# Kernel tuning notes

Measured on AMD Instinct MI355X. Metric: run time of the kernel, lower is better.

Reference implementation:

```python
import jax, jax.numpy as jnp
import numpy as np

B, S, D = 4, 8192, 512
WS = 512        # window_size
LB = 1          # look_backward (look_forward = 0, causal)


def setup_inputs() -> dict:
    key = jax.random.key(0)
    k1, k2, k3 = jax.random.split(key, 3)
    text = jax.random.normal(k1, (B, S, D), dtype=jnp.float32)
    audio = jax.random.normal(k2, (B, S, D), dtype=jnp.float32)
    video = jax.random.normal(k3, (B, S, D), dtype=jnp.float32)
    return {"text": text, "audio": audio, "video": video}


def _local_attention(q, k, v, ws=WS, lb=LB):
    # q, k, v: [b, n, d]; sliding-window causal attention, each query window
    # attends to its own window plus `lb` previous windows.
    b, n, d = q.shape
    w = n // ws
    scale = d ** -0.5
    qw = q.reshape(b, w, ws, d) * scale
    kw = k.reshape(b, w, ws, d)
    vw = v.reshape(b, w, ws, d)

    def look_around(x):
        # pad lb windows of zeros at the front, gather lb+1 shifted views
        padded = jnp.pad(x, ((0, 0), (lb, 0), (0, 0), (0, 0)))
        return jnp.concatenate([padded[:, i:i + w] for i in range(lb + 1)], axis=2)

    kk = look_around(kw)  # [b, w, (lb+1)*ws, d]
    vv = look_around(vw)

    # absolute positions for causal + padding mask
    t = jnp.arange(n).reshape(w, ws)                        # query positions [w, ws]
    tk = jnp.pad(t, ((lb, 0), (0, 0)), constant_values=-1)  # pad windows get -1
    bq_k = jnp.concatenate([tk[i:i + w] for i in range(lb + 1)], axis=1)  # [w, (lb+1)*ws]
    mask = (t[:, :, None] >= bq_k[:, None, :]) & (bq_k[:, None, :] >= 0)  # [w, ws, (lb+1)*ws]

    sim = jnp.einsum('bwid,bwjd->bwij', qw, kk)             # [b, w, ws, (lb+1)*ws]
    sim = jnp.where(mask[None], sim, jnp.finfo(sim.dtype).min)
    attn = jax.nn.softmax(sim, axis=-1)
    out = jnp.einsum('bwij,bwjd->bwid', attn, vv)
    return out.reshape(b, n, d)


def reference(text, audio, video):
    # GATSBlock.forward: x = self.local_attn(text, audio, video)
    # i.e. q = text, k = audio, v = video (modalities pre-projected to [b, n, d])
    return _local_attention(text, audio, video)
```

## Files before the change

kernel.cpp:

```cpp
#include <hip/hip_runtime.h>
#include <hip/hip_bf16.h>

#define S_ 8192
#define D_ 512
#define WSZ 512
#define QBLK 64
#define KBLK 32
#define ATT_THREADS 256
#define PSTRIDE 2560
#define ATT_LDS (65536 + 2 * PSTRIDE)

using bf16x8 = __attribute__((ext_vector_type(8))) __bf16;
using f32x4  = __attribute__((ext_vector_type(4))) float;
using f32x16 = __attribute__((ext_vector_type(16))) float;

#define GLDS(gp, lp) __builtin_amdgcn_global_load_lds( \
    (const __attribute__((address_space(1))) void*)(gp), \
    (__attribute__((address_space(3))) void*)(lp), 16, 0, 0)

__global__ __launch_bounds__(256) void cvt_k(const float* __restrict__ in,
                                             ushort* __restrict__ out) {
    const int bid = blockIdx.x;
    const int j = bid & 7, t = (bid >> 3) & 255, b = bid >> 11;
    const int u = j * 256 + threadIdx.x;
    const int c = u >> 7, row = (u >> 2) & 31, h = u & 3;
    const float* src = in + ((size_t)(b * S_ + t * 32 + row)) * D_ + c * 32 + h * 8;
    float4 a0 = *(const float4*)(src);
    float4 a1 = *(const float4*)(src + 4);
    bf16x8 o;
    o[0] = (__bf16)a0.x; o[1] = (__bf16)a0.y; o[2] = (__bf16)a0.z; o[3] = (__bf16)a0.w;
    o[4] = (__bf16)a1.x; o[5] = (__bf16)a1.y; o[6] = (__bf16)a1.z; o[7] = (__bf16)a1.w;
    *(bf16x8*)(out + (size_t)(b * 256 + t) * 16384 + u * 8) = o;
}

__global__ __launch_bounds__(256) void tr_v(const float* __restrict__ V,
                                            char* __restrict__ Vt) {
    __shared__ float tile[64][68];
    const int bid = blockIdx.x;
    const int d0 = (bid & 7) * 64;
    const int s0 = ((bid >> 3) & 127) * 64;
    const int b  = bid >> 10;
    const int t  = threadIdx.x;
    {
        const int sl = t >> 2, cg = (t & 3) * 16;
        const float* src = V + ((size_t)b * S_ + s0 + sl) * D_ + d0 + cg;
        #pragma unroll
        for (int j = 0; j < 4; ++j)
            *(float4*)&tile[sl][cg + j * 4] = *(const float4*)(src + j * 4);
    }
    __syncthreads();
    {
        const int dl = t >> 2, sg = (t & 3) * 16;
        const int d  = d0 + dl;
        const int tt = (s0 + sg) >> 5;
        const int kk = (s0 + sg) & 31;
        bf16x8 o0, o1;
        #pragma unroll
        for (int j = 0; j < 8; ++j) {
            o0[j] = (__bf16)tile[sg + j][dl];
            o1[j] = (__bf16)tile[sg + 8 + j][dl];
        }
        char* base = Vt + (size_t)(b * 256 + tt) * 32768 +
                     (d >> 5) * 2048 + (d & 31) * 16;
        *(bf16x8*)(base + (kk >> 4) * 1024)       = o0;
        *(bf16x8*)(base + (kk >> 4) * 1024 + 512) = o1;
    }
}

__global__ __launch_bounds__(ATT_THREADS, 2) void gats_attn(
    const float* __restrict__ Qg, const char* __restrict__ Kbg,
    const char* __restrict__ Vtg, float* __restrict__ Og)
{
    extern __shared__ char smem[];
    const int tid  = threadIdx.x;
    const int lane = tid & 63;
    const int wv   = tid >> 6;
    const int h    = lane >> 4;
    const int lq   = lane & 15;
    const int hh   = lane >> 5;
    const int l31  = lane & 31;
    const int u    = wv & 1;
    const int pr   = wv >> 1;
    char* Pp = smem + 65536 + pr * PSTRIDE;
    char* Pf = Pp + 2048;
    const int laneK = lq * 64 + h * 16;

    const int bid = blockIdx.x;
    const int r2  = bid >> 3;
    const int w   = (bid & 7) * 2 + (r2 & 1);
    const int b   = (r2 >> 1) & 3;
    const int y   = r2 >> 3;
    const int qbase    = w * WSZ + y * QBLK;
    const int pairbase = qbase + pr * 32;
    const int wqbase   = qbase + wv * 16;

    const float* Qp  = Qg  + (size_t)b * S_ * D_;
    const char*  Kbp = Kbg + (size_t)b * 256 * 32768;
    const char*  Vtp = Vtg + (size_t)b * 256 * 32768;
    float*       Op  = Og  + (size_t)b * S_ * D_;

    const float scale = 0.044194173824159216f;
    const float L2E   = 1.44269504088896f;

    bf16x8 qf[16];
    {
        const int qrow = wqbase + lq;
        const float* qsrc = Qp + (size_t)qrow * D_ + h * 8;
        #pragma unroll
        for (int c = 0; c < 16; ++c) {
            float4 a0 = *(const float4*)(qsrc + c * 32);
            float4 a1 = *(const float4*)(qsrc + c * 32 + 4);
            bf16x8 q;
            q[0] = (__bf16)(a0.x * scale); q[1] = (__bf16)(a0.y * scale);
            q[2] = (__bf16)(a0.z * scale); q[3] = (__bf16)(a0.w * scale);
            q[4] = (__bf16)(a1.x * scale); q[5] = (__bf16)(a1.y * scale);
            q[6] = (__bf16)(a1.z * scale); q[7] = (__bf16)(a1.w * scale);
            qf[c] = q;
        }
    }

    f32x16 acc[8];
    #pragma unroll
    for (int dt = 0; dt < 8; ++dt)
        #pragma unroll
        for (int rg = 0; rg < 16; ++rg) acc[dt][rg] = 0.f;
    float m_run = -1e30f, l_run = 0.f;

    const int kstart = (w == 0) ? 0 : (w - 1) * WSZ;
    const int ktend  = qbase + QBLK;

    auto STAGE = [&](int kt) {
        char* kb = smem;
        char* vb = smem + 32768;
        const size_t tb = ((size_t)(kt >> 5)) << 15;
        const char* ksrc = Kbp + tb;
        const char* vsrc = Vtp + tb;
        #pragma unroll
        for (int s2 = 0; s2 < 8; ++s2) {
            const int off = wv * 8192 + s2 * 1024;
            GLDS(ksrc + off + lane * 16, kb + off);
            GLDS(vsrc + off + lane * 16, vb + off);
        }
    };

    STAGE(kstart);
    for (int kt = kstart; kt < ktend; kt += KBLK) {
        asm volatile("s_waitcnt vmcnt(0)" ::: "memory");
        __builtin_amdgcn_s_barrier();

        const bool active = (kt <= pairbase + 31);
        char* Ksh = smem;
        char* Vsh = smem + 32768;

        if (active) {
            f32x4 st[2];
            __builtin_amdgcn_s_setprio(1);
            #pragma unroll
            for (int g = 0; g < 2; ++g) {
                f32x4 sa = (f32x4){0.f, 0.f, 0.f, 0.f};
                f32x4 sb = (f32x4){0.f, 0.f, 0.f, 0.f};
                #pragma unroll
                for (int c = 0; c < 16; ++c) {
                    const int byte = c * 2048 + g * 1024 + laneK;
                    bf16x8 kf = *(const bf16x8*)(Ksh + byte);
                    if (c & 1) sb = __builtin_amdgcn_mfma_f32_16x16x32_bf16(kf, qf[c], sb, 0, 0, 0);
                    else       sa = __builtin_amdgcn_mfma_f32_16x16x32_bf16(kf, qf[c], sa, 0, 0, 0);
                }
                st[g] = sa + sb;
            }
            __builtin_amdgcn_s_setprio(0);

            const int qg = wqbase + lq;
            if (kt + 31 > wqbase) {
                #pragma unroll
                for (int g = 0; g < 2; ++g)
                    #pragma unroll
                    for (int r = 0; r < 4; ++r) {
                        const int key = kt + g * 16 + h * 4 + r;
                        if (key > qg) st[g][r] = -1e30f;
                    }
            }

            float own = fmaxf(fmaxf(fmaxf(st[0][0], st[0][1]), fmaxf(st[0][2], st[0][3])),
                              fmaxf(fmaxf(st[1][0], st[1][1]), fmaxf(st[1][2], st[1][3])));
            float tmax = fmaxf(own, __shfl_xor(own, 16));
            tmax = fmaxf(tmax, __shfl_xor(tmax, 32));

            const bool anyneed = __any(tmax > m_run + 8.f);
            float f_val = 1.0f;
            if (anyneed) {
                const float mnew = fmaxf(m_run, tmax);
                f_val = exp2f((m_run - mnew) * L2E);
                m_run = mnew;
                l_run *= f_val;
            }

            const float p00 = exp2f((st[0][0] - m_run) * L2E);
            const float p01 = exp2f((st[0][1] - m_run) * L2E);
            const float p02 = exp2f((st[0][2] - m_run) * L2E);
            const float p03 = exp2f((st[0][3] - m_run) * L2E);
            const float p10 = exp2f((st[1][0] - m_run) * L2E);
            const float p11 = exp2f((st[1][1] - m_run) * L2E);
            const float p12 = exp2f((st[1][2] - m_run) * L2E);
            const float p13 = exp2f((st[1][3] - m_run) * L2E);
            float rs = p00 + p01 + p02 + p03 + p10 + p11 + p12 + p13;
            rs += __shfl_xor(rs, 16);
            rs += __shfl_xor(rs, 32);
            l_run += rs;

            uint c0, c1, c2, c3;
            asm("v_cvt_pk_bf16_f32 %0, %1, %2" : "=v"(c0) : "v"(p00), "v"(p01));
            asm("v_cvt_pk_bf16_f32 %0, %1, %2" : "=v"(c1) : "v"(p02), "v"(p03));
            asm("v_cvt_pk_bf16_f32 %0, %1, %2" : "=v"(c2) : "v"(p10), "v"(p11));
            asm("v_cvt_pk_bf16_f32 %0, %1, %2" : "=v"(c3) : "v"(p12), "v"(p13));
            const int wbase = (h >> 1) * 512 + (h & 1) * 8 + (u * 16 + lq) * 16;
            *(uint*)(Pp + wbase)            = c0;
            *(uint*)(Pp + wbase + 4)        = c1;
            *(uint*)(Pp + 1024 + wbase)     = c2;
            *(uint*)(Pp + 1024 + wbase + 4) = c3;
            if (h == 0)    *(float*)(Pf + (u * 16 + lq) * 4) = f_val;
            if (lane == 0) *(uint*)(Pf + 128 + u * 4) = anyneed ? 1u : 0u;
        }

        asm volatile("s_waitcnt lgkmcnt(0)" ::: "memory");
        __builtin_amdgcn_sched_barrier(0);
        __builtin_amdgcn_s_barrier();

        if (active) {
            const uint2 fl = *(const uint2*)(Pf + 128);
            if (fl.x | fl.y) {
                f32x4 fr[4];
                #pragma unroll
                for (int i = 0; i < 4; ++i)
                    fr[i] = *(const f32x4*)(Pf + i * 32 + hh * 16);
                #pragma unroll
                for (int dt = 0; dt < 8; ++dt)
                    #pragma unroll
                    for (int rg = 0; rg < 16; ++rg)
                        acc[dt][rg] *= fr[rg >> 2][rg & 3];
            }

            bf16x8 pa0 = *(const bf16x8*)(Pp + hh * 512 + l31 * 16);
            bf16x8 pa1 = *(const bf16x8*)(Pp + 1024 + hh * 512 + l31 * 16);
            __builtin_amdgcn_s_setprio(1);
            #pragma unroll
            for (int dt = 0; dt < 8; ++dt) {
                const int vb = (u * 8 + dt) * 2048 + hh * 512 + l31 * 16;
                bf16x8 v0 = *(const bf16x8*)(Vsh + vb);
                bf16x8 v1 = *(const bf16x8*)(Vsh + vb + 1024);
                acc[dt] = __builtin_amdgcn_mfma_f32_32x32x16_bf16(pa0, v0, acc[dt], 0, 0, 0);
                acc[dt] = __builtin_amdgcn_mfma_f32_32x32x16_bf16(pa1, v1, acc[dt], 0, 0, 0);
            }
            __builtin_amdgcn_s_setprio(0);
        }
        __builtin_amdgcn_s_barrier();
        if (kt + KBLK < ktend) STAGE(kt + KBLK);
    }

    if (h == 0) *(float*)(Pf + (u * 16 + lq) * 4) = l_run;
    asm volatile("s_waitcnt lgkmcnt(0)" ::: "memory");
    __builtin_amdgcn_s_barrier();
    f32x4 iv[4];
    #pragma unroll
    for (int i = 0; i < 4; ++i) {
        f32x4 lv = *(const f32x4*)(Pf + i * 32 + hh * 16);
        iv[i][0] = 1.0f / lv[0]; iv[i][1] = 1.0f / lv[1];
        iv[i][2] = 1.0f / lv[2]; iv[i][3] = 1.0f / lv[3];
    }
    #pragma unroll
    for (int dt = 0; dt < 8; ++dt) {
        const int colb = u * 256 + dt * 32 + l31;
        #pragma unroll
        for (int rg = 0; rg < 16; ++rg) {
            const int row = pairbase + (rg & 3) + 8 * (rg >> 2) + 4 * hh;
            Op[(size_t)row * D_ + colb] = acc[dt][rg] * iv[rg >> 2][rg & 3];
        }
    }
}

#define FB_LDS (32768 + 32768 + 4 * 1024)
__global__ __launch_bounds__(256, 2) void gats_attn_fb(
    const float* __restrict__ Qg, const float* __restrict__ Kg,
    const float* __restrict__ Vg, float* __restrict__ Og)
{
    extern __shared__ char smem[];
    char* Ksh = smem;
    char* Vsh = smem + 32768;
    const int tid  = threadIdx.x;
    const int lane = tid & 63;
    const int wv   = tid >> 6;
    char* Psh = smem + 65536 + wv * 1024;
    const int bid = blockIdx.x;
    const int wh  = bid & 7;
    const int r2  = bid >> 3;
    const int w   = wh * 2 + (r2 & 1);
    const int b   = (r2 >> 1) & 3;
    const int y   = r2 >> 3;
    const int qbase  = w * WSZ + y * 64;
    const int wqbase = qbase + wv * 16;
    const size_t boff = (size_t)b * S_ * D_;
    const float* Qp = Qg + boff; const float* Kp = Kg + boff;
    const float* Vp = Vg + boff; float* Op = Og + boff;
    const float scale = 0.044194173824159216f;
    const float L2E   = 1.44269504088896f;
    bf16x8 qf[16];
    {
        const int qrow = wqbase + (lane & 15);
        const float* qsrc = Qp + (size_t)qrow * D_ + ((lane >> 4) * 8);
        #pragma unroll
        for (int c = 0; c < 16; ++c) {
            float4 a0 = *(const float4*)(qsrc + c * 32);
            float4 a1 = *(const float4*)(qsrc + c * 32 + 4);
            bf16x8 q;
            q[0] = (__bf16)(a0.x * scale); q[1] = (__bf16)(a0.y * scale);
            q[2] = (__bf16)(a0.z * scale); q[3] = (__bf16)(a0.w * scale);
            q[4] = (__bf16)(a1.x * scale); q[5] = (__bf16)(a1.y * scale);
            q[6] = (__bf16)(a1.z * scale); q[7] = (__bf16)(a1.w * scale);
            qf[c] = q;
        }
    }
    f32x4 acc[32];
    #pragma unroll
    for (int i = 0; i < 32; ++i) acc[i] = (f32x4){0.f, 0.f, 0.f, 0.f};
    float m_r[4], l_r[4];
    #pragma unroll
    for (int r = 0; r < 4; ++r) { m_r[r] = -1e30f; l_r[r] = 0.f; }
    const int kstart = (w == 0) ? 0 : (w - 1) * WSZ;
    const int ktend  = qbase + 64;
    for (int kt = kstart; kt < ktend; kt += 32) {
        __syncthreads();
        #pragma unroll
        for (int s = 0; s < 8; ++s) {
            const int row = s * 4 + wv;
            const int dof = lane * 8;
            const float4* src = (const float4*)(Kp + (size_t)(kt + row) * D_ + dof);
            float4 a0 = src[0], a1 = src[1];
            bf16x8 kv;
            kv[0] = (__bf16)a0.x; kv[1] = (__bf16)a0.y; kv[2] = (__bf16)a0.z; kv[3] = (__bf16)a0.w;
            kv[4] = (__bf16)a1.x; kv[5] = (__bf16)a1.y; kv[6] = (__bf16)a1.z; kv[7] = (__bf16)a1.w;
            const int byte = row * 1024 + ((dof * 2) ^ ((row & 7) << 4));
            *(bf16x8*)(Ksh + byte) = kv;
        }
        #pragma unroll
        for (int hh2 = 0; hh2 < 2; ++hh2) {
            const int d = tid + hh2 * 256;
            #pragma unroll
            for (int it = 0; it < 4; ++it) {
                float vvv[8];
                #pragma unroll
                for (int j = 0; j < 8; ++j)
                    vvv[j] = Vp[(size_t)(kt + it * 8 + j) * D_ + d];
                bf16x8 vb;
                #pragma unroll
                for (int j = 0; j < 8; ++j) vb[j] = (__bf16)vvv[j];
                const int byte = d * 64 + ((it * 16) ^ (((d >> 1) & 3) << 4));
                *(bf16x8*)(Vsh + byte) = vb;
            }
        }
        __syncthreads();
        if (kt > wqbase + 15) continue;
        f32x4 sacc[2];
        #pragma unroll
        for (int g = 0; g < 2; ++g) {
            f32x4 s = (f32x4){0.f, 0.f, 0.f, 0.f};
            const int keyrow = g * 16 + (lane & 15);
            #pragma unroll
            for (int c = 0; c < 16; ++c) {
                const int byte = keyrow * 1024 +
                                 ((c * 64 + (lane >> 4) * 16) ^ ((keyrow & 7) << 4));
                bf16x8 kf = *(const bf16x8*)(Ksh + byte);
                s = __builtin_amdgcn_mfma_f32_16x16x32_bf16(qf[c], kf, s, 0, 0, 0);
            }
            sacc[g] = s;
        }
        #pragma unroll
        for (int g = 0; g < 2; ++g) {
            if (kt + g * 16 + 15 > wqbase) {
                const int kg = kt + g * 16 + (lane & 15);
                #pragma unroll
                for (int r = 0; r < 4; ++r) {
                    const int qrow = wqbase + (lane >> 4) * 4 + r;
                    if (kg > qrow) sacc[g][r] = -1e30f;
                }
            }
        }
        float tmax[4];
        #pragma unroll
        for (int r = 0; r < 4; ++r) {
            float v = fmaxf(sacc[0][r], sacc[1][r]);
            #pragma unroll
            for (int off = 8; off >= 1; off >>= 1)
                v = fmaxf(v, __shfl_xor(v, off));
            tmax[r] = v;
        }
        bool need = false;
        #pragma unroll
        for (int r = 0; r < 4; ++r) need |= (tmax[r] > m_r[r] + 8.f);
        if (__any(need)) {
            #pragma unroll
            for (int r = 0; r < 4; ++r) {
                const float mnew = fmaxf(m_r[r], tmax[r]);
                const float f = exp2f((m_r[r] - mnew) * L2E);
                m_r[r] = mnew; l_r[r] *= f;
                #pragma unroll
                for (int dc = 0; dc < 32; ++dc) acc[dc][r] *= f;
            }
        }
        float rsum[4] = {0.f, 0.f, 0.f, 0.f};
        #pragma unroll
        for (int g = 0; g < 2; ++g) {
            #pragma unroll
            for (int r = 0; r < 4; ++r) {
                const float p = exp2f((sacc[g][r] - m_r[r]) * L2E);
                rsum[r] += p;
                const int prow = (lane >> 4) * 4 + r;
                const int byte = prow * 64 +
                                 ((g * 32 + (lane & 15) * 2) ^ (((prow >> 1) & 3) << 4));
                *(__bf16*)(Psh + byte) = (__bf16)p;
            }
        }
        #pragma unroll
        for (int r = 0; r < 4; ++r) {
            float v = rsum[r];
            #pragma unroll
            for (int off = 8; off >= 1; off >>= 1)
                v += __shfl_xor(v, off);
            l_r[r] += v;
        }
        {
            const int prow  = lane & 15;
            const int pbyte = prow * 64 +
                              (((lane >> 4) * 16) ^ (((prow >> 1) & 3) << 4));
            bf16x8 pa = *(const bf16x8*)(Psh + pbyte);
            #pragma unroll
            for (int dc = 0; dc < 32; ++dc) {
                const int d = dc * 16 + (lane & 15);
                const int vbyte = d * 64 +
                                  (((lane >> 4) * 16) ^ (((d >> 1) & 3) << 4));
                bf16x8 vf = *(const bf16x8*)(Vsh + vbyte);
                acc[dc] = __builtin_amdgcn_mfma_f32_16x16x32_bf16(pa, vf, acc[dc], 0, 0, 0);
            }
        }
    }
    float inv[4];
    #pragma unroll
    for (int r = 0; r < 4; ++r) inv[r] = 1.0f / l_r[r];
    #pragma unroll
    for (int dc = 0; dc < 32; ++dc) {
        #pragma unroll
        for (int r = 0; r < 4; ++r) {
            const int row = wqbase + (lane >> 4) * 4 + r;
            const int col = dc * 16 + (lane & 15);
            Op[(size_t)row * D_ + col] = acc[dc][r] * inv[r];
        }
    }
}

extern "C" void kernel_launch(void* const* d_in, const int* in_sizes, int n_in,
                              void* d_out, int out_size, void* d_ws, size_t ws_size,
                              hipStream_t stream) {
    const float* q = (const float*)d_in[0];
    const float* k = (const float*)d_in[1];
    const float* v = (const float*)d_in[2];
    float* o = (float*)d_out;

    const size_t elems = (size_t)4 * S_ * D_ * 4;
    const size_t need  = elems * 2 * 2;
    if (ws_size >= need) {
        char* kb = (char*)d_ws;
        char* vt = (char*)d_ws + elems * 2;
        cvt_k<<<dim3(8192), dim3(256), 0, stream>>>(k, (ushort*)kb);
        tr_v <<<dim3(4096), dim3(256), 0, stream>>>(v, vt);
        hipFuncSetAttribute((const void*)gats_attn,
                            hipFuncAttributeMaxDynamicSharedMemorySize, ATT_LDS);
        gats_attn<<<dim3(512), dim3(ATT_THREADS), ATT_LDS, stream>>>(q, kb, vt, o);
    } else {
        hipFuncSetAttribute((const void*)gats_attn_fb,
                            hipFuncAttributeMaxDynamicSharedMemorySize, FB_LDS);
        gats_attn_fb<<<dim3(512), dim3(256), FB_LDS, stream>>>(q, k, v, o);
    }
}
```

Measured before the change: 149.3 us.

## Double query and key tile sizes with register-prefetched K/V staging

```diff
diff --git a/kernel.cpp b/kernel.cpp
--- a/kernel.cpp
+++ b/kernel.cpp
@@ -4,11 +4,11 @@
 #define S_ 8192
 #define D_ 512
 #define WSZ 512
-#define QBLK 64
-#define KBLK 32
-#define ATT_THREADS 256
-#define PSTRIDE 2560
-#define ATT_LDS (65536 + 2 * PSTRIDE)
+#define QBLK 128
+#define KBLK 64
+#define ATT_THREADS 512
+#define PSTRIDE 4608
+#define ATT_LDS (131072 + 4 * PSTRIDE)
 
 using bf16x8 = __attribute__((ext_vector_type(8))) __bf16;
 using f32x4  = __attribute__((ext_vector_type(4))) float;
@@ -72,6 +72,7 @@
     const char* __restrict__ Vtg, float* __restrict__ Og)
 {
     extern __shared__ char smem[];
+    char* Vsh = smem + 65536;
     const int tid  = threadIdx.x;
     const int lane = tid & 63;
     const int wv   = tid >> 6;
@@ -81,8 +82,8 @@
     const int l31  = lane & 31;
     const int u    = wv & 1;
     const int pr   = wv >> 1;
-    char* Pp = smem + 65536 + pr * PSTRIDE;
-    char* Pf = Pp + 2048;
+    char* Pp = smem + 131072 + pr * PSTRIDE;
+    char* Pf = Pp + 4096;
     const int laneK = lq * 64 + h * 16;
 
     const int bid = blockIdx.x;
@@ -129,40 +130,41 @@
     const int kstart = (w == 0) ? 0 : (w - 1) * WSZ;
     const int ktend  = qbase + QBLK;
 
-    auto STAGE = [&](int kt) {
-        char* kb = smem;
-        char* vb = smem + 32768;
-        const size_t tb = ((size_t)(kt >> 5)) << 15;
-        const char* ksrc = Kbp + tb;
-        const char* vsrc = Vtp + tb;
-        #pragma unroll
-        for (int s2 = 0; s2 < 8; ++s2) {
-            const int off = wv * 8192 + s2 * 1024;
-            GLDS(ksrc + off + lane * 16, kb + off);
-            GLDS(vsrc + off + lane * 16, vb + off);
-        }
-    };
-
-    STAGE(kstart);
+    {
+        const size_t tb = ((size_t)(kstart >> 5)) << 15;
+        #pragma unroll
+        for (int i = 0; i < 8; ++i) {
+            const int off = i * 8192 + wv * 1024;
+            GLDS(Kbp + tb + off + lane * 16, smem + off);
+            GLDS(Vtp + tb + off + lane * 16, Vsh + off);
+        }
+    }
+    float4 sf[16];
+    {
+        const size_t tb = ((size_t)((kstart + KBLK) >> 5)) << 15;
+        #pragma unroll
+        for (int i = 0; i < 8; ++i) {
+            sf[i]     = *(const float4*)(Kbp + tb + i * 8192 + tid * 16);
+            sf[8 + i] = *(const float4*)(Vtp + tb + i * 8192 + tid * 16);
+        }
+    }
+    asm volatile("s_waitcnt vmcnt(16)" ::: "memory");
+    __builtin_amdgcn_s_barrier();
+
     for (int kt = kstart; kt < ktend; kt += KBLK) {
-        asm volatile("s_waitcnt vmcnt(0)" ::: "memory");
-        __builtin_amdgcn_s_barrier();
-
         const bool active = (kt <= pairbase + 31);
-        char* Ksh = smem;
-        char* Vsh = smem + 32768;
 
         if (active) {
-            f32x4 st[2];
+            f32x4 st[4];
             __builtin_amdgcn_s_setprio(1);
             #pragma unroll
-            for (int g = 0; g < 2; ++g) {
+            for (int g = 0; g < 4; ++g) {
                 f32x4 sa = (f32x4){0.f, 0.f, 0.f, 0.f};
                 f32x4 sb = (f32x4){0.f, 0.f, 0.f, 0.f};
                 #pragma unroll
                 for (int c = 0; c < 16; ++c) {
-                    const int byte = c * 2048 + g * 1024 + laneK;
-                    bf16x8 kf = *(const bf16x8*)(Ksh + byte);
+                    const int byte = (g >> 1) * 32768 + c * 2048 + (g & 1) * 1024 + laneK;
+                    bf16x8 kf = *(const bf16x8*)(smem + byte);
                     if (c & 1) sb = __builtin_amdgcn_mfma_f32_16x16x32_bf16(kf, qf[c], sb, 0, 0, 0);
                     else       sa = __builtin_amdgcn_mfma_f32_16x16x32_bf16(kf, qf[c], sa, 0, 0, 0);
                 }
@@ -171,9 +173,9 @@
             __builtin_amdgcn_s_setprio(0);
 
             const int qg = wqbase + lq;
-            if (kt + 31 > wqbase) {
-                #pragma unroll
-                for (int g = 0; g < 2; ++g)
+            if (kt + 63 > wqbase) {
+                #pragma unroll
+                for (int g = 0; g < 4; ++g)
                     #pragma unroll
                     for (int r = 0; r < 4; ++r) {
                         const int key = kt + g * 16 + h * 4 + r;
@@ -181,8 +183,11 @@
                     }
             }
 
-            float own = fmaxf(fmaxf(fmaxf(st[0][0], st[0][1]), fmaxf(st[0][2], st[0][3])),
-                              fmaxf(fmaxf(st[1][0], st[1][1]), fmaxf(st[1][2], st[1][3])));
+            float own = -1e30f;
+            #pragma unroll
+            for (int g = 0; g < 4; ++g)
+                #pragma unroll
+                for (int r = 0; r < 4; ++r) own = fmaxf(own, st[g][r]);
             float tmax = fmaxf(own, __shfl_xor(own, 16));
             tmax = fmaxf(tmax, __shfl_xor(tmax, 32));
 
@@ -195,29 +200,32 @@
                 l_run *= f_val;
             }
 
-            const float p00 = exp2f((st[0][0] - m_run) * L2E);
-            const float p01 = exp2f((st[0][1] - m_run) * L2E);
-            const float p02 = exp2f((st[0][2] - m_run) * L2E);
-            const float p03 = exp2f((st[0][3] - m_run) * L2E);
-            const float p10 = exp2f((st[1][0] - m_run) * L2E);
-            const float p11 = exp2f((st[1][1] - m_run) * L2E);
-            const float p12 = exp2f((st[1][2] - m_run) * L2E);
-            const float p13 = exp2f((st[1][3] - m_run) * L2E);
-            float rs = p00 + p01 + p02 + p03 + p10 + p11 + p12 + p13;
+            float p[4][4];
+            float rs = 0.f;
+            #pragma unroll
+            for (int g = 0; g < 4; ++g)
+                #pragma unroll
+                for (int r = 0; r < 4; ++r) {
+                    const float v = exp2f((st[g][r] - m_run) * L2E);
+                    p[g][r] = v;
+                    rs += v;
+                }
             rs += __shfl_xor(rs, 16);
             rs += __shfl_xor(rs, 32);
             l_run += rs;
 
-            uint c0, c1, c2, c3;
-            asm("v_cvt_pk_bf16_f32 %0, %1, %2" : "=v"(c0) : "v"(p00), "v"(p01));
-            asm("v_cvt_pk_bf16_f32 %0, %1, %2" : "=v"(c1) : "v"(p02), "v"(p03));
-            asm("v_cvt_pk_bf16_f32 %0, %1, %2" : "=v"(c2) : "v"(p10), "v"(p11));
-            asm("v_cvt_pk_bf16_f32 %0, %1, %2" : "=v"(c3) : "v"(p12), "v"(p13));
+            uint cA[4], cB[4];
+            #pragma unroll
+            for (int g = 0; g < 4; ++g) {
+                asm("v_cvt_pk_bf16_f32 %0, %1, %2" : "=v"(cA[g]) : "v"(p[g][0]), "v"(p[g][1]));
+                asm("v_cvt_pk_bf16_f32 %0, %1, %2" : "=v"(cB[g]) : "v"(p[g][2]), "v"(p[g][3]));
+            }
             const int wbase = (h >> 1) * 512 + (h & 1) * 8 + (u * 16 + lq) * 16;
-            *(uint*)(Pp + wbase)            = c0;
-            *(uint*)(Pp + wbase + 4)        = c1;
-            *(uint*)(Pp + 1024 + wbase)     = c2;
-            *(uint*)(Pp + 1024 + wbase + 4) = c3;
+            #pragma unroll
+            for (int g = 0; g < 4; ++g) {
+                *(uint*)(Pp + g * 1024 + wbase)     = cA[g];
+                *(uint*)(Pp + g * 1024 + wbase + 4) = cB[g];
+            }
             if (h == 0)    *(float*)(Pf + (u * 16 + lq) * 4) = f_val;
             if (lane == 0) *(uint*)(Pf + 128 + u * 4) = anyneed ? 1u : 0u;
         }
@@ -240,21 +248,40 @@
                         acc[dt][rg] *= fr[rg >> 2][rg & 3];
             }
 
-            bf16x8 pa0 = *(const bf16x8*)(Pp + hh * 512 + l31 * 16);
-            bf16x8 pa1 = *(const bf16x8*)(Pp + 1024 + hh * 512 + l31 * 16);
+            bf16x8 pa[4];
+            #pragma unroll
+            for (int ks = 0; ks < 4; ++ks)
+                pa[ks] = *(const bf16x8*)(Pp + ks * 1024 + hh * 512 + l31 * 16);
             __builtin_amdgcn_s_setprio(1);
             #pragma unroll
             for (int dt = 0; dt < 8; ++dt) {
-                const int vb = (u * 8 + dt) * 2048 + hh * 512 + l31 * 16;
-                bf16x8 v0 = *(const bf16x8*)(Vsh + vb);
-                bf16x8 v1 = *(const bf16x8*)(Vsh + vb + 1024);
-                acc[dt] = __builtin_amdgcn_mfma_f32_32x32x16_bf16(pa0, v0, acc[dt], 0, 0, 0);
-                acc[dt] = __builtin_amdgcn_mfma_f32_32x32x16_bf16(pa1, v1, acc[dt], 0, 0, 0);
+                #pragma unroll
+                for (int ks = 0; ks < 4; ++ks) {
+                    const int vb = (ks >> 1) * 32768 + (u * 8 + dt) * 2048 +
+                                   (ks & 1) * 1024 + hh * 512 + l31 * 16;
+                    bf16x8 vf = *(const bf16x8*)(Vsh + vb);
+                    acc[dt] = __builtin_amdgcn_mfma_f32_32x32x16_bf16(pa[ks], vf, acc[dt], 0, 0, 0);
+                }
             }
             __builtin_amdgcn_s_setprio(0);
         }
         __builtin_amdgcn_s_barrier();
-        if (kt + KBLK < ktend) STAGE(kt + KBLK);
+
+        if (kt + KBLK < ktend) {
+            #pragma unroll
+            for (int i = 0; i < 16; ++i)
+                *(float4*)(smem + i * 8192 + tid * 16) = sf[i];
+            if (kt + 2 * KBLK < ktend) {
+                const size_t tb = ((size_t)((kt + 2 * KBLK) >> 5)) << 15;
+                #pragma unroll
+                for (int i = 0; i < 8; ++i) {
+                    sf[i]     = *(const float4*)(Kbp + tb + i * 8192 + tid * 16);
+                    sf[8 + i] = *(const float4*)(Vtp + tb + i * 8192 + tid * 16);
+                }
+            }
+            asm volatile("s_waitcnt lgkmcnt(0)" ::: "memory");
+            __builtin_amdgcn_s_barrier();
+        }
     }
 
     if (h == 0) *(float*)(Pf + (u * 16 + lq) * 4) = l_run;
@@ -473,7 +500,7 @@
         tr_v <<<dim3(4096), dim3(256), 0, stream>>>(v, vt);
         hipFuncSetAttribute((const void*)gats_attn,
                             hipFuncAttributeMaxDynamicSharedMemorySize, ATT_LDS);
-        gats_attn<<<dim3(512), dim3(ATT_THREADS), ATT_LDS, stream>>>(q, kb, vt, o);
+        gats_attn<<<dim3(256), dim3(ATT_THREADS), ATT_LDS, stream>>>(q, kb, vt, o);
     } else {
         hipFuncSetAttribute((const void*)gats_attn_fb,
                             hipFuncAttributeMaxDynamicSharedMemorySize, FB_LDS);
```

Result: slower. 289.6 us (+93.9%).
